# Performance work log

Hardware: AMD Instinct MI355X
Metric: run time of the kernel (lower is better)

Reference implementation:

```python
import jax, jax.numpy as jnp
import numpy as np

N = 100000      # nodes
E = 1600000     # edges
R = 8           # relations
D_IN = 64
D_H = 64
D_OUT = 64
G = 64          # graphs in batch


def setup_inputs() -> dict:
    key = jax.random.key(0)
    ks = jax.random.split(key, 10)
    x = jax.random.normal(ks[0], (N, D_IN), dtype=jnp.float32)
    edge_index = jax.random.randint(ks[1], (2, E), 0, N, dtype=jnp.int32)
    edge_type = jax.random.randint(ks[2], (E,), 0, R, dtype=jnp.int32)
    batch = jnp.sort(jax.random.randint(ks[3], (N,), 0, G, dtype=jnp.int32))
    s1 = 1.0 / np.sqrt(D_IN)
    s2 = 1.0 / np.sqrt(D_H)
    W1 = jax.random.normal(ks[4], (R, D_IN, D_H), dtype=jnp.float32) * s1
    root1 = jax.random.normal(ks[5], (D_IN, D_H), dtype=jnp.float32) * s1
    b1 = jnp.zeros((D_H,), dtype=jnp.float32)
    W2 = jax.random.normal(ks[6], (R, D_H, D_OUT), dtype=jnp.float32) * s2
    root2 = jax.random.normal(ks[7], (D_H, D_OUT), dtype=jnp.float32) * s2
    b2 = jnp.zeros((D_OUT,), dtype=jnp.float32)
    return {"x": x, "edge_index": edge_index, "edge_type": edge_type, "batch": batch,
            "W1": W1, "root1": root1, "b1": b1, "W2": W2, "root2": root2, "b2": b2}


def _rgcn_conv(x, src, dst, etype, W, root, b):
    # PyG RGCNConv (num_bases=None, aggr='mean'):
    #   out_i = sum_r mean_{j in N_r(i)} x_j @ W_r + x_i @ root + b
    # Aggregate-then-transform: per-(dst, relation) mean of source features,
    # then one einsum over relation weights.
    num_nodes, d = x.shape
    num_rel = W.shape[0]
    seg = dst * num_rel + etype                          # composite (node, rel) id
    sums = jax.ops.segment_sum(x[src], seg, num_segments=num_nodes * num_rel)
    cnt = jax.ops.segment_sum(jnp.ones_like(seg, dtype=x.dtype), seg,
                              num_segments=num_nodes * num_rel)
    mean = sums / jnp.maximum(cnt, 1.0)[:, None]         # [N*R, d]
    mean = mean.reshape(num_nodes, num_rel, d)           # [N, R, d]
    return jnp.einsum('nrd,rdh->nh', mean, W) + x @ root + b


def reference(x, edge_index, edge_type, batch, W1, root1, b1, W2, root2, b2):
    src, dst = edge_index[0], edge_index[1]
    h = jax.nn.relu(_rgcn_conv(x, src, dst, edge_type, W1, root1, b1))
    h = _rgcn_conv(h, src, dst, edge_type, W2, root2, b2)
    # global_mean_pool over graph ids
    gsum = jax.ops.segment_sum(h, batch, num_segments=G)
    gcnt = jax.ops.segment_sum(jnp.ones((h.shape[0],), h.dtype), batch, num_segments=G)
    return gsum / jnp.maximum(gcnt, 1.0)[:, None]
```

## Files before the change

### kernel.cpp

```cpp
#include <hip/hip_runtime.h>
#include <stdint.h>

typedef __attribute__((ext_vector_type(8))) short short8;
typedef __attribute__((ext_vector_type(4))) float floatx4;
typedef __attribute__((ext_vector_type(4))) unsigned short ushort4v;

__device__ inline float bf2f(unsigned short u) {
  union { unsigned int i; float f; } v; v.i = ((unsigned int)u) << 16; return v.f;
}
__device__ inline unsigned short f2bf(float f) {
  union { float f; unsigned int i; } v; v.f = f;
  unsigned int r = v.i + 0x7FFFu + ((v.i >> 16) & 1u);
  return (unsigned short)(r >> 16);
}

__global__ void conv_prep(const float* __restrict__ W1, const float* __restrict__ root1,
                          const float* __restrict__ W2, const float* __restrict__ root2,
                          unsigned short* __restrict__ Wb, int* __restrict__ cnt, int n2)
{
  int i = blockIdx.x * blockDim.x + threadIdx.x;
  if (i < 2 * 9 * 4096) {
    int layer = i / 36864;
    int rem = i - layer * 36864;
    int m = rem >> 12, rem2 = rem & 4095, k = rem2 >> 6, c = rem2 & 63;
    const float* Wm = layer ? W2 : W1;
    const float* rt = layer ? root2 : root1;
    float w = (m < 8) ? Wm[(size_t)m * 4096 + k * 64 + c] : rt[(size_t)k * 64 + c];
    int kc = k >> 5, q = (k >> 3) & 3, j = k & 7, nt = c >> 4, lcv = c & 15;
    Wb[(size_t)(layer * 9 + m) * 4096 + (size_t)(((kc * 4 + q) * 4 + nt) * 16 + lcv) * 8 + j] = f2bf(w);
  } else {
    int z = i - 2 * 9 * 4096;
    if (z < n2) cnt[z] = 0;
  }
}

__device__ __forceinline__ void transform_tile(
    int t, int N, int lane, const float* __restrict__ X, int relu,
    const unsigned short* __restrict__ Wb, const float* __restrict__ bias,
    unsigned short* __restrict__ Y, float* __restrict__ accR)
{
  const int lc = lane & 15, quad = lane >> 4;
  const int nb = t << 4;
  const int row = min(nb + lc, N - 1);
  const float* xr = X + (size_t)row * 64;
  short8 a0, a1;
#pragma unroll
  for (int j = 0; j < 8; ++j) {
    float v0 = xr[quad * 8 + j];
    float v1 = xr[32 + quad * 8 + j];
    if (relu) { v0 = fmaxf(v0, 0.f); v1 = fmaxf(v1, 0.f); }
    a0[j] = (short)f2bf(v0);
    a1[j] = (short)f2bf(v1);
  }
#pragma unroll
  for (int g = 0; g < 9; ++g) {
#pragma unroll
    for (int nt = 0; nt < 4; ++nt) {
      const short8 b0 = *(const short8*)&Wb[(size_t)g * 4096 +
          (size_t)(((0 * 4 + quad) * 4 + nt) * 16 + lc) * 8];
      const short8 b1 = *(const short8*)&Wb[(size_t)g * 4096 +
          (size_t)(((1 * 4 + quad) * 4 + nt) * 16 + lc) * 8];
      floatx4 d = {0.f, 0.f, 0.f, 0.f};
      d = __builtin_amdgcn_mfma_f32_16x16x32_bf16(a0, b0, d, 0, 0, 0);
      d = __builtin_amdgcn_mfma_f32_16x16x32_bf16(a1, b1, d, 0, 0, 0);
      const int c = nt * 16 + lc;
      if (g < 8) {
#pragma unroll
        for (int i = 0; i < 4; ++i) {
          int r_ = nb + quad * 4 + i;
          if (r_ < N) Y[(size_t)r_ * 512 + g * 64 + c] = f2bf(d[i]);
        }
      } else {
        const float bv = bias[c];
#pragma unroll
        for (int i = 0; i < 4; ++i) {
          int r_ = nb + quad * 4 + i;
          if (r_ < N) accR[(size_t)r_ * 64 + c] = d[i] + bv;
        }
      }
    }
  }
}

__global__ void __launch_bounds__(256)
count_and_t1(const int* __restrict__ dst, const int* __restrict__ et,
             int* __restrict__ cnt, unsigned short* __restrict__ rank, int E,
             const float* __restrict__ x, const unsigned short* __restrict__ Wb1,
             const float* __restrict__ b1, unsigned short* __restrict__ Y,
             float* __restrict__ accA, int N, int TB)
{
  const unsigned bx = blockIdx.x;
  const bool isT = (bx % 5u == 0u) && (bx / 5u < (unsigned)TB);
  if (isT) {
    const int lane = threadIdx.x & 63;
    const int wave = threadIdx.x >> 6;
    const int t = (int)(bx / 5u) * 4 + wave;
    if (t < ((N + 15) >> 4))
      transform_tile(t, N, lane, x, 0, Wb1, b1, Y, accA);
  } else {
    const unsigned nT = min((bx + 4u) / 5u, (unsigned)TB);
    const int e = (int)(bx - nT) * 256 + (int)threadIdx.x;
    if (e < E) {
      int idx = dst[e] * 8 + et[e];
      rank[e] = (unsigned short)atomicAdd(&cnt[idx], 1);
    }
  }
}

__global__ void __launch_bounds__(256)
transform_l2(const float* __restrict__ accA, const unsigned short* __restrict__ Wb2,
             const float* __restrict__ b2, unsigned short* __restrict__ Y,
             float* __restrict__ accB, int N)
{
  const int lane = threadIdx.x & 63;
  const int wave = threadIdx.x >> 6;
  const int t = blockIdx.x * 4 + wave;
  if (t < ((N + 15) >> 4))
    transform_tile(t, N, lane, accA, 1, Wb2, b2, Y, accB);
}

#define SCAN_T 256
#define SCAN_E 4

__global__ void scan1(const int* __restrict__ cnt, int* __restrict__ bsum, int n) {
  __shared__ int lds[SCAN_T];
  int base = blockIdx.x * (SCAN_T * SCAN_E);
  int tid = threadIdx.x;
  int s = 0;
#pragma unroll
  for (int j = 0; j < SCAN_E; ++j) {
    int i = base + tid * SCAN_E + j;
    if (i < n) s += cnt[i];
  }
  lds[tid] = s; __syncthreads();
  for (int off = SCAN_T / 2; off > 0; off >>= 1) {
    if (tid < off) lds[tid] += lds[tid + off];
    __syncthreads();
  }
  if (tid == 0) bsum[blockIdx.x] = lds[0];
}

__global__ void scan2(int* __restrict__ bsum, int* __restrict__ eptr, int nb, int n) {
  __shared__ int lds[SCAN_T];
  int tid = threadIdx.x;
  int loc[4]; int s = 0;
#pragma unroll
  for (int j = 0; j < 4; ++j) {
    int i = tid * 4 + j;
    loc[j] = (i < nb) ? bsum[i] : 0; s += loc[j];
  }
  lds[tid] = s; __syncthreads();
  for (int off = 1; off < SCAN_T; off <<= 1) {
    int v = (tid >= off) ? lds[tid - off] : 0;
    __syncthreads();
    lds[tid] += v;
    __syncthreads();
  }
  int run = (tid > 0 ? lds[tid - 1] : 0);
#pragma unroll
  for (int j = 0; j < 4; ++j) {
    int i = tid * 4 + j;
    if (i < nb) { int v = loc[j]; bsum[i] = run; run += v; }
  }
  if (tid == 0) eptr[n] = lds[SCAN_T - 1];
}

__global__ void scan3(const int* __restrict__ cnt, const int* __restrict__ bsum,
                      int* __restrict__ eptr, int n) {
  __shared__ int lds[SCAN_T];
  int base = blockIdx.x * (SCAN_T * SCAN_E);
  int tid = threadIdx.x;
  int loc[SCAN_E]; int s = 0;
#pragma unroll
  for (int j = 0; j < SCAN_E; ++j) {
    int i = base + tid * SCAN_E + j;
    loc[j] = (i < n) ? cnt[i] : 0; s += loc[j];
  }
  lds[tid] = s; __syncthreads();
  for (int off = 1; off < SCAN_T; off <<= 1) {
    int v = (tid >= off) ? lds[tid - off] : 0;
    __syncthreads();
    lds[tid] += v;
    __syncthreads();
  }
  int run = (tid > 0 ? lds[tid - 1] : 0) + bsum[blockIdx.x];
#pragma unroll
  for (int j = 0; j < SCAN_E; ++j) {
    int i = base + tid * SCAN_E + j;
    if (i < n) { eptr[i] = run; run += loc[j]; }
  }
}

__global__ void scatter_edges(const int* __restrict__ src, const int* __restrict__ dst,
                              const int* __restrict__ et, const int* __restrict__ eptr8,
                              const unsigned short* __restrict__ rank,
                              unsigned* __restrict__ entry, int E) {
  int e = blockIdx.x * blockDim.x + threadIdx.x;
  if (e < E) {
    int d = dst[e], r = et[e];
    int p = eptr8[d * 8 + r] + (int)rank[e];
    entry[p] = ((unsigned)src[e] << 3) | (unsigned)r;
  }
}

__global__ void __launch_bounds__(256)
edge_agg_csr(const unsigned short* __restrict__ Y, const int* __restrict__ eptr8,
             const unsigned* __restrict__ entry, float* __restrict__ acc, int N)
{
  const int wid  = (blockIdx.x * blockDim.x + threadIdx.x) >> 6;
  const int lane = threadIdx.x & 63;
  if (wid >= N) return;
  const int bv = eptr8[wid * 8 + (lane < 9 ? lane : 8)];
  const int lo = __shfl(bv, 0), hi = __shfl(bv, 8);
  const int wdt = __shfl(bv, (lane & 7) + 1) - __shfl(bv, lane & 7);
  const float invv = 1.0f / (float)max(wdt, 1);

  const int half = lane >> 5;
  const int sub  = lane & 31;
  float s0 = 0.f, s1 = 0.f;

#define GATHER2(ename, vname, wname, pidx)                                     \
  unsigned ename = __shfl(en, 2 * (pidx) + half);                              \
  unsigned vname = *(const unsigned*)&Y[(size_t)(ename >> 3) * 512 +           \
                                        (ename & 7) * 64 + sub * 2];           \
  float wname = __shfl(invv, (int)(ename & 7));

  for (int base = lo; base < hi; base += 64) {
    const int rem = hi - base;
    const int mm = rem < 64 ? rem : 64;
    const unsigned en = entry[base + (lane < mm ? lane : mm - 1)];
    const int pairs = mm >> 1;
    int i = 0;
    for (; i + 8 <= pairs; i += 8) {
      GATHER2(ea, va, wa, i)     GATHER2(eb, vb, wb, i + 1)
      GATHER2(ec, vc, wc, i + 2) GATHER2(ed, vd, wd, i + 3)
      GATHER2(ee, ve, we, i + 4) GATHER2(ef, vf, wf, i + 5)
      GATHER2(eg, vg, wg, i + 6) GATHER2(eh, vh, wh, i + 7)
      s0 += bf2f((unsigned short)(va & 0xffff)) * wa + bf2f((unsigned short)(vb & 0xffff)) * wb
          + bf2f((unsigned short)(vc & 0xffff)) * wc + bf2f((unsigned short)(vd & 0xffff)) * wd
          + bf2f((unsigned short)(ve & 0xffff)) * we + bf2f((unsigned short)(vf & 0xffff)) * wf
          + bf2f((unsigned short)(vg & 0xffff)) * wg + bf2f((unsigned short)(vh & 0xffff)) * wh;
      s1 += bf2f((unsigned short)(va >> 16)) * wa + bf2f((unsigned short)(vb >> 16)) * wb
          + bf2f((unsigned short)(vc >> 16)) * wc + bf2f((unsigned short)(vd >> 16)) * wd
          + bf2f((unsigned short)(ve >> 16)) * we + bf2f((unsigned short)(vf >> 16)) * wf
          + bf2f((unsigned short)(vg >> 16)) * wg + bf2f((unsigned short)(vh >> 16)) * wh;
    }
    for (; i < pairs; ++i) {
      GATHER2(ea, va, wa, i)
      s0 += bf2f((unsigned short)(va & 0xffff)) * wa;
      s1 += bf2f((unsigned short)(va >> 16)) * wa;
    }
    if (mm & 1) {
      unsigned e0 = __shfl(en, mm - 1);
      float w0 = __shfl(invv, (int)(e0 & 7));
      if (lane < 32) {
        unsigned v = *(const unsigned*)&Y[(size_t)(e0 >> 3) * 512 + (e0 & 7) * 64 + sub * 2];
        s0 += bf2f((unsigned short)(v & 0xffff)) * w0;
        s1 += bf2f((unsigned short)(v >> 16)) * w0;
      }
    }
  }
#undef GATHER2
  float a0 = __shfl(s0, lane >> 1);
  float a1 = __shfl(s1, lane >> 1);
  float b0 = __shfl(s0, 32 + (lane >> 1));
  float b1 = __shfl(s1, 32 + (lane >> 1));
  float sum = ((lane & 1) ? a1 : a0) + ((lane & 1) ? b1 : b0);
  acc[(size_t)wid * 64 + lane] += sum;
}

__device__ inline int lbound(const int* __restrict__ batch, int Nn, int g) {
  int lo = 0, hi = Nn;
  while (lo < hi) { int m = (lo + hi) >> 1; if (batch[m] < g) lo = m + 1; else hi = m; }
  return lo;
}

#define PS 24
__global__ void __launch_bounds__(256)
pool1(const float* __restrict__ acc, const int* __restrict__ batch,
      float* __restrict__ partial, int N, int G)
{
  const int g = blockIdx.x;
  const int s = blockIdx.y;
  const int lane = threadIdx.x & 63;
  const int w = threadIdx.x >> 6;
  const int lo = lbound(batch, N, g);
  const int hi = lbound(batch, N, g + 1);
  const int len = hi - lo;
  const int a = lo + (int)(((long long)len * s) / PS);
  const int b = lo + (int)(((long long)len * (s + 1)) / PS);
  float sum = 0.f;
  for (int n = a + w; n < b; n += 4) sum += acc[(size_t)n * 64 + lane];
  __shared__ float red[4][64];
  red[w][lane] = sum;
  __syncthreads();
  if (w == 0)
    partial[((size_t)g * PS + s) * 64 + lane] =
        red[0][lane] + red[1][lane] + red[2][lane] + red[3][lane];
}

__global__ void pool2(const float* __restrict__ partial, const int* __restrict__ batch,
                      float* __restrict__ out, int N, int G)
{
  const int g = blockIdx.x;
  const int lane = threadIdx.x;
  float t = 0.f;
#pragma unroll
  for (int s = 0; s < PS; ++s) t += partial[((size_t)g * PS + s) * 64 + lane];
  const int len = lbound(batch, N, g + 1) - lbound(batch, N, g);
  out[(size_t)g * 64 + lane] = t / fmaxf((float)len, 1.0f);
}

extern "C" void kernel_launch(void* const* d_in, const int* in_sizes, int n_in,
                              void* d_out, int out_size, void* d_ws, size_t ws_size,
                              hipStream_t stream)
{
  const float* x     = (const float*)d_in[0];
  const int*   ei    = (const int*)d_in[1];
  const int*   etype = (const int*)d_in[2];
  const int*   batch = (const int*)d_in[3];
  const float* W1    = (const float*)d_in[4];
  const float* root1 = (const float*)d_in[5];
  const float* b1    = (const float*)d_in[6];
  const float* W2    = (const float*)d_in[7];
  const float* root2 = (const float*)d_in[8];
  const float* b2    = (const float*)d_in[9];

  const int N = in_sizes[0] / 64;
  const int E = in_sizes[1] / 2;
  const int R = in_sizes[4] / (64 * 64);
  const int G = out_size / 64;
  const int* srcp = ei;
  const int* dstp = ei + E;
  const int n2 = N * R;

  char* ws = (char*)d_ws;
  size_t off = 0;
  auto carve = [&](size_t bytes) -> void* {
    void* p = ws + off; off = (off + bytes + 255) & ~(size_t)255; return p;
  };
  float*          accA    = (float*)carve((size_t)N * 64 * 4);
  float*          accB    = (float*)carve((size_t)N * 64 * 4);
  unsigned short* Y       = (unsigned short*)carve((size_t)N * R * 64 * 2);
  int*            eptr8   = (int*)carve((size_t)(n2 + 1) * 4);
  unsigned*       entry   = (unsigned*)carve((size_t)E * 4);
  int*            bsum    = (int*)carve(1024 * 4);
  float*          partial = (float*)carve((size_t)G * PS * 64 * 4);
  unsigned short* Wb      = (unsigned short*)carve((size_t)2 * 9 * 4096 * 2);
  int*            cnt  = (int*)accB;
  unsigned short* rank = (unsigned short*)((char*)accB + ((size_t)4 << 20));
  (void)ws_size; (void)n_in;

  const int nb2 = (n2 + SCAN_T * SCAN_E - 1) / (SCAN_T * SCAN_E);
  const int tiles = (N + 15) >> 4;
  const int TB = (tiles + 3) / 4;
  const int CB = (E + 255) / 256;
  const int prep_total = 2 * 9 * 4096 + n2;

  conv_prep<<<(prep_total + 255) / 256, 256, 0, stream>>>(W1, root1, W2, root2, Wb, cnt, n2);

  count_and_t1<<<CB + TB, 256, 0, stream>>>(dstp, etype, cnt, rank, E,
                                            x, Wb, b1, Y, accA, N, TB);

  scan1<<<nb2, SCAN_T, 0, stream>>>(cnt, bsum, n2);
  scan2<<<1, SCAN_T, 0, stream>>>(bsum, eptr8, nb2, n2);
  scan3<<<nb2, SCAN_T, 0, stream>>>(cnt, bsum, eptr8, n2);
  scatter_edges<<<(E + 255) / 256, 256, 0, stream>>>(srcp, dstp, etype, eptr8, rank, entry, E);

  const int aggBlocks = (N * 64 + 255) / 256;

  edge_agg_csr<<<aggBlocks, 256, 0, stream>>>(Y, eptr8, entry, accA, N);

  transform_l2<<<TB, 256, 0, stream>>>(accA, Wb + 9 * 4096, b2, Y, accB, N);
  edge_agg_csr<<<aggBlocks, 256, 0, stream>>>(Y, eptr8, entry, accB, N);

  dim3 pgrid(G, PS);
  pool1<<<pgrid, 256, 0, stream>>>(accB, batch, partial, N, G);
  pool2<<<G, 64, 0, stream>>>(partial, batch, (float*)d_out, N, G);
}
```

Measured before the change: 399.4 us.

## Fuse scan and edge scatter into one kernel with grid barriers

Replaces the three scan kernels and the scatter kernel with a single persistent kernel that separates phases using a software grid barrier (an atomic counter that is reset in conv_prep). This removes three kernel launches and their gaps. The edge-aggregation gather loop is also unrolled to 16 pairs, with a 4-pair tail, to keep more loads in flight. The barrier assumes all nb2 (~782) blocks are co-resident, and it adds spin-wait cost on the atomic.

```diff
diff --git a/kernel.cpp b/kernel.cpp
--- a/kernel.cpp
+++ b/kernel.cpp
@@ -13,10 +13,13 @@
   unsigned int r = v.i + 0x7FFFu + ((v.i >> 16) & 1u);
   return (unsigned short)(r >> 16);
 }
+__device__ inline float blo(unsigned v) { return bf2f((unsigned short)(v & 0xffff)); }
+__device__ inline float bhi(unsigned v) { return bf2f((unsigned short)(v >> 16)); }
 
 __global__ void conv_prep(const float* __restrict__ W1, const float* __restrict__ root1,
                           const float* __restrict__ W2, const float* __restrict__ root2,
-                          unsigned short* __restrict__ Wb, int* __restrict__ cnt, int n2)
+                          unsigned short* __restrict__ Wb, int* __restrict__ cnt,
+                          int* __restrict__ bar, int n2)
 {
   int i = blockIdx.x * blockDim.x + threadIdx.x;
   if (i < 2 * 9 * 4096) {
@@ -31,6 +34,7 @@
   } else {
     int z = i - 2 * 9 * 4096;
     if (z < n2) cnt[z] = 0;
+    else if (z == n2) *bar = 0;
   }
 }
 
@@ -119,36 +123,73 @@
     transform_tile(t, N, lane, accA, 1, Wb2, b2, Y, accB);
 }
 
+__device__ inline void grid_barrier(int* bar, int target) {
+  __syncthreads();
+  if (threadIdx.x == 0) {
+    __threadfence();
+    atomicAdd(bar, 1);
+    while (atomicAdd(bar, 0) < target) {}
+  }
+  __syncthreads();
+  __threadfence();
+}
+
 #define SCAN_T 256
 #define SCAN_E 4
-
-__global__ void scan1(const int* __restrict__ cnt, int* __restrict__ bsum, int n) {
+__global__ void __launch_bounds__(256)
+csr_scan_scatter(const int* __restrict__ cnt, int* __restrict__ bsum,
+                 int* __restrict__ eptr8, int* __restrict__ bar,
+                 const int* __restrict__ src, const int* __restrict__ dst,
+                 const int* __restrict__ et, const unsigned short* __restrict__ rank,
+                 unsigned* __restrict__ entry, int n, int E, int NB)
+{
   __shared__ int lds[SCAN_T];
-  int base = blockIdx.x * (SCAN_T * SCAN_E);
-  int tid = threadIdx.x;
-  int s = 0;
+  __shared__ int bbase;
+  const int tid = threadIdx.x;
+  const int bid = (int)blockIdx.x;
+  const int base = bid * (SCAN_T * SCAN_E);
+
+  int loc[SCAN_E]; int s = 0;
 #pragma unroll
   for (int j = 0; j < SCAN_E; ++j) {
     int i = base + tid * SCAN_E + j;
-    if (i < n) s += cnt[i];
+    loc[j] = (i < n) ? cnt[i] : 0; s += loc[j];
   }
   lds[tid] = s; __syncthreads();
   for (int off = SCAN_T / 2; off > 0; off >>= 1) {
     if (tid < off) lds[tid] += lds[tid + off];
     __syncthreads();
   }
-  if (tid == 0) bsum[blockIdx.x] = lds[0];
-}
-
-__global__ void scan2(int* __restrict__ bsum, int* __restrict__ eptr, int nb, int n) {
-  __shared__ int lds[SCAN_T];
-  int tid = threadIdx.x;
-  int loc[4]; int s = 0;
-#pragma unroll
-  for (int j = 0; j < 4; ++j) {
-    int i = tid * 4 + j;
-    loc[j] = (i < nb) ? bsum[i] : 0; s += loc[j];
-  }
+  if (tid == 0) bsum[bid] = lds[0];
+
+  grid_barrier(bar, NB);
+
+  if (bid == 0) {
+    int l2[4]; int s2 = 0;
+#pragma unroll
+    for (int j = 0; j < 4; ++j) {
+      int i = tid * 4 + j;
+      l2[j] = (i < NB) ? bsum[i] : 0; s2 += l2[j];
+    }
+    lds[tid] = s2; __syncthreads();
+    for (int off = 1; off < SCAN_T; off <<= 1) {
+      int v = (tid >= off) ? lds[tid - off] : 0;
+      __syncthreads();
+      lds[tid] += v;
+      __syncthreads();
+    }
+    int run = (tid > 0 ? lds[tid - 1] : 0);
+#pragma unroll
+    for (int j = 0; j < 4; ++j) {
+      int i = tid * 4 + j;
+      if (i < NB) { int v = l2[j]; bsum[i] = run; run += v; }
+    }
+    if (tid == 0) eptr8[n] = lds[SCAN_T - 1];
+  }
+
+  grid_barrier(bar, 2 * NB);
+
+  if (tid == 0) bbase = atomicAdd(&bsum[bid], 0);
   lds[tid] = s; __syncthreads();
   for (int off = 1; off < SCAN_T; off <<= 1) {
     int v = (tid >= off) ? lds[tid - off] : 0;
@@ -156,47 +197,16 @@
     lds[tid] += v;
     __syncthreads();
   }
-  int run = (tid > 0 ? lds[tid - 1] : 0);
-#pragma unroll
-  for (int j = 0; j < 4; ++j) {
-    int i = tid * 4 + j;
-    if (i < nb) { int v = loc[j]; bsum[i] = run; run += v; }
-  }
-  if (tid == 0) eptr[n] = lds[SCAN_T - 1];
-}
-
-__global__ void scan3(const int* __restrict__ cnt, const int* __restrict__ bsum,
-                      int* __restrict__ eptr, int n) {
-  __shared__ int lds[SCAN_T];
-  int base = blockIdx.x * (SCAN_T * SCAN_E);
-  int tid = threadIdx.x;
-  int loc[SCAN_E]; int s = 0;
+  int run = (tid > 0 ? lds[tid - 1] : 0) + bbase;
 #pragma unroll
   for (int j = 0; j < SCAN_E; ++j) {
     int i = base + tid * SCAN_E + j;
-    loc[j] = (i < n) ? cnt[i] : 0; s += loc[j];
-  }
-  lds[tid] = s; __syncthreads();
-  for (int off = 1; off < SCAN_T; off <<= 1) {
-    int v = (tid >= off) ? lds[tid - off] : 0;
-    __syncthreads();
-    lds[tid] += v;
-    __syncthreads();
-  }
-  int run = (tid > 0 ? lds[tid - 1] : 0) + bsum[blockIdx.x];
-#pragma unroll
-  for (int j = 0; j < SCAN_E; ++j) {
-    int i = base + tid * SCAN_E + j;
-    if (i < n) { eptr[i] = run; run += loc[j]; }
-  }
-}
-
-__global__ void scatter_edges(const int* __restrict__ src, const int* __restrict__ dst,
-                              const int* __restrict__ et, const int* __restrict__ eptr8,
-                              const unsigned short* __restrict__ rank,
-                              unsigned* __restrict__ entry, int E) {
-  int e = blockIdx.x * blockDim.x + threadIdx.x;
-  if (e < E) {
+    if (i < n) { eptr8[i] = run; run += loc[j]; }
+  }
+
+  grid_barrier(bar, 3 * NB);
+
+  for (int e = bid * SCAN_T + tid; e < E; e += NB * SCAN_T) {
     int d = dst[e], r = et[e];
     int p = eptr8[d * 8 + r] + (int)rank[e];
     entry[p] = ((unsigned)src[e] << 3) | (unsigned)r;
@@ -231,32 +241,42 @@
     const unsigned en = entry[base + (lane < mm ? lane : mm - 1)];
     const int pairs = mm >> 1;
     int i = 0;
-    for (; i + 8 <= pairs; i += 8) {
+    for (; i + 16 <= pairs; i += 16) {
+      GATHER2(eA, vA, wA, i)      GATHER2(eB, vB, wB, i + 1)
+      GATHER2(eC, vC, wC, i + 2)  GATHER2(eD, vD, wD, i + 3)
+      GATHER2(eE, vE, wE, i + 4)  GATHER2(eF, vF, wF, i + 5)
+      GATHER2(eG, vG, wG, i + 6)  GATHER2(eH, vH, wH, i + 7)
+      GATHER2(eI, vI, wI, i + 8)  GATHER2(eJ, vJ, wJ, i + 9)
+      GATHER2(eK, vK, wK, i + 10) GATHER2(eL, vL, wL, i + 11)
+      GATHER2(eM, vM, wM, i + 12) GATHER2(eN, vN, wN, i + 13)
+      GATHER2(eO, vO, wO, i + 14) GATHER2(eP, vP, wP, i + 15)
+      s0 += blo(vA) * wA + blo(vB) * wB + blo(vC) * wC + blo(vD) * wD
+          + blo(vE) * wE + blo(vF) * wF + blo(vG) * wG + blo(vH) * wH
+          + blo(vI) * wI + blo(vJ) * wJ + blo(vK) * wK + blo(vL) * wL
+          + blo(vM) * wM + blo(vN) * wN + blo(vO) * wO + blo(vP) * wP;
+      s1 += bhi(vA) * wA + bhi(vB) * wB + bhi(vC) * wC + bhi(vD) * wD
+          + bhi(vE) * wE + bhi(vF) * wF + bhi(vG) * wG + bhi(vH) * wH
+          + bhi(vI) * wI + bhi(vJ) * wJ + bhi(vK) * wK + bhi(vL) * wL
+          + bhi(vM) * wM + bhi(vN) * wN + bhi(vO) * wO + bhi(vP) * wP;
+    }
+    for (; i + 4 <= pairs; i += 4) {
       GATHER2(ea, va, wa, i)     GATHER2(eb, vb, wb, i + 1)
       GATHER2(ec, vc, wc, i + 2) GATHER2(ed, vd, wd, i + 3)
-      GATHER2(ee, ve, we, i + 4) GATHER2(ef, vf, wf, i + 5)
-      GATHER2(eg, vg, wg, i + 6) GATHER2(eh, vh, wh, i + 7)
-      s0 += bf2f((unsigned short)(va & 0xffff)) * wa + bf2f((unsigned short)(vb & 0xffff)) * wb
-          + bf2f((unsigned short)(vc & 0xffff)) * wc + bf2f((unsigned short)(vd & 0xffff)) * wd
-          + bf2f((unsigned short)(ve & 0xffff)) * we + bf2f((unsigned short)(vf & 0xffff)) * wf
-          + bf2f((unsigned short)(vg & 0xffff)) * wg + bf2f((unsigned short)(vh & 0xffff)) * wh;
-      s1 += bf2f((unsigned short)(va >> 16)) * wa + bf2f((unsigned short)(vb >> 16)) * wb
-          + bf2f((unsigned short)(vc >> 16)) * wc + bf2f((unsigned short)(vd >> 16)) * wd
-          + bf2f((unsigned short)(ve >> 16)) * we + bf2f((unsigned short)(vf >> 16)) * wf
-          + bf2f((unsigned short)(vg >> 16)) * wg + bf2f((unsigned short)(vh >> 16)) * wh;
+      s0 += blo(va) * wa + blo(vb) * wb + blo(vc) * wc + blo(vd) * wd;
+      s1 += bhi(va) * wa + bhi(vb) * wb + bhi(vc) * wc + bhi(vd) * wd;
     }
     for (; i < pairs; ++i) {
       GATHER2(ea, va, wa, i)
-      s0 += bf2f((unsigned short)(va & 0xffff)) * wa;
-      s1 += bf2f((unsigned short)(va >> 16)) * wa;
+      s0 += blo(va) * wa;
+      s1 += bhi(va) * wa;
     }
     if (mm & 1) {
       unsigned e0 = __shfl(en, mm - 1);
       float w0 = __shfl(invv, (int)(e0 & 7));
       if (lane < 32) {
         unsigned v = *(const unsigned*)&Y[(size_t)(e0 >> 3) * 512 + (e0 & 7) * 64 + sub * 2];
-        s0 += bf2f((unsigned short)(v & 0xffff)) * w0;
-        s1 += bf2f((unsigned short)(v >> 16)) * w0;
+        s0 += blo(v) * w0;
+        s1 += bhi(v) * w0;
       }
     }
   }
@@ -345,6 +365,7 @@
   int*            eptr8   = (int*)carve((size_t)(n2 + 1) * 4);
   unsigned*       entry   = (unsigned*)carve((size_t)E * 4);
   int*            bsum    = (int*)carve(1024 * 4);
+  int*            bar     = (int*)carve(256);
   float*          partial = (float*)carve((size_t)G * PS * 64 * 4);
   unsigned short* Wb      = (unsigned short*)carve((size_t)2 * 9 * 4096 * 2);
   int*            cnt  = (int*)accB;
@@ -355,17 +376,15 @@
   const int tiles = (N + 15) >> 4;
   const int TB = (tiles + 3) / 4;
   const int CB = (E + 255) / 256;
-  const int prep_total = 2 * 9 * 4096 + n2;
-
-  conv_prep<<<(prep_total + 255) / 256, 256, 0, stream>>>(W1, root1, W2, root2, Wb, cnt, n2);
+  const int prep_total = 2 * 9 * 4096 + n2 + 1;
+
+  conv_prep<<<(prep_total + 255) / 256, 256, 0, stream>>>(W1, root1, W2, root2, Wb, cnt, bar, n2);
 
   count_and_t1<<<CB + TB, 256, 0, stream>>>(dstp, etype, cnt, rank, E,
                                             x, Wb, b1, Y, accA, N, TB);
 
-  scan1<<<nb2, SCAN_T, 0, stream>>>(cnt, bsum, n2);
-  scan2<<<1, SCAN_T, 0, stream>>>(bsum, eptr8, nb2, n2);
-  scan3<<<nb2, SCAN_T, 0, stream>>>(cnt, bsum, eptr8, n2);
-  scatter_edges<<<(E + 255) / 256, 256, 0, stream>>>(srcp, dstp, etype, eptr8, rank, entry, E);
+  csr_scan_scatter<<<nb2, SCAN_T, 0, stream>>>(cnt, bsum, eptr8, bar,
+                                               srcp, dstp, etype, rank, entry, n2, E, nb2);
 
   const int aggBlocks = (N * 64 + 255) / 256;
 
```

After: 716.8 us. 79.5% more time.
